# Kernel optimization log

Hardware: AMD Instinct MI355X
Metric: run time of the kernel (lower is better)

Reference implementation:

```python
import jax, jax.numpy as jnp
import numpy as np

N = 100_000
E = 1_600_000
IN_DIM = 3
HID = 64
NUM_CLASSES = 3
BN_EPS = 1e-5


def setup_inputs() -> dict:
    key = jax.random.key(0)
    ks = jax.random.split(key, 16)
    x = jax.random.normal(ks[0], (N, IN_DIM), dtype=jnp.float32)
    row = jax.random.randint(ks[1], (E,), 0, N, dtype=jnp.int32)
    col = jax.random.randint(ks[2], (E,), 0, N, dtype=jnp.int32)
    vals = jax.random.uniform(ks[3], (E,), dtype=jnp.float32)
    # parameters
    W1 = jax.random.normal(ks[4], (IN_DIM, HID), dtype=jnp.float32) / np.sqrt(IN_DIM)
    b1 = jnp.zeros((HID,), jnp.float32)
    W2 = jax.random.normal(ks[5], (HID, HID), dtype=jnp.float32) / np.sqrt(HID)
    b2 = jnp.zeros((HID,), jnp.float32)
    g1 = jnp.ones((HID,), jnp.float32)
    be1 = jnp.zeros((HID,), jnp.float32)
    m1 = jax.random.normal(ks[6], (HID,), dtype=jnp.float32) * 0.1
    v1 = jax.random.uniform(ks[7], (HID,), dtype=jnp.float32) + 0.5
    g2 = jnp.ones((HID,), jnp.float32)
    be2 = jnp.zeros((HID,), jnp.float32)
    m2 = jax.random.normal(ks[8], (HID,), dtype=jnp.float32) * 0.1
    v2 = jax.random.uniform(ks[9], (HID,), dtype=jnp.float32) + 0.5
    Wc = jax.random.normal(ks[10], (2 * HID, NUM_CLASSES), dtype=jnp.float32) / np.sqrt(2 * HID)
    bc = jnp.zeros((NUM_CLASSES,), jnp.float32)
    return dict(x=x, row=row, col=col, vals=vals, W1=W1, b1=b1, g1=g1, be1=be1,
                m1=m1, v1=v1, W2=W2, b2=b2, g2=g2, be2=be2, m2=m2, v2=v2,
                Wc=Wc, bc=bc)


def _spmm(row, col, vals, h):
    # sparse [N,N] @ dense [N,H] via gather + segment_sum
    return jax.ops.segment_sum(vals[:, None] * h[col], row, num_segments=N)


def _bn_eval(h, g, be, m, v):
    return (h - m) * jax.lax.rsqrt(v + BN_EPS) * g + be


def reference(x, row, col, vals, W1, b1, g1, be1, m1, v1,
              W2, b2, g2, be2, m2, v2, Wc, bc):
    h = _spmm(row, col, vals, x @ W1 + b1)          # [N, HID]
    h = jax.nn.relu(_bn_eval(h, g1, be1, m1, v1))   # eval: dropout no-op
    h = _spmm(row, col, vals, h @ W2 + b2)          # [N, HID]
    h = jax.nn.relu(_bn_eval(h, g2, be2, m2, v2))
    g = jnp.concatenate([h.mean(axis=0), h.max(axis=0)], axis=0)  # [2*HID]
    return g @ Wc + bc                               # [NUM_CLASSES]
```

## Files before the change

### kernel.cpp

```cpp
#include <hip/hip_runtime.h>
#include <hip/hip_bf16.h>

#define HID 64
#define BN_EPS 1e-5f
#define BROWS 256
#define MAXB 512
#define BCAP 4608
#define BATCH 4096
#define S2STRIDE 4096

typedef __attribute__((ext_vector_type(8))) short bf16x8;
typedef __attribute__((ext_vector_type(4))) float f32x4;

__global__ __launch_bounds__(512) void zero_bcur_k(int* __restrict__ bcur,
                                                   int* __restrict__ fincnt) {
  bcur[threadIdx.x] = 0;
  if (threadIdx.x == 0) *fincnt = 0;
}

__global__ __launch_bounds__(256) void bucketA_k(
    const int* __restrict__ row, const int* __restrict__ col,
    const float* __restrict__ vals, int* __restrict__ bcur,
    int2* __restrict__ bucketed, int E, int NB) {
  __shared__ int cnt[MAXB];
  __shared__ int scn[MAXB];
  __shared__ int cnt2[MAXB];
  __shared__ int gbase[MAXB];
  __shared__ int2 stg[BATCH];
  __shared__ unsigned short stgb[BATCH];
  int t = threadIdx.x;
  int start = blockIdx.x * BATCH;
  for (int i = t; i < MAXB; i += 256) cnt[i] = 0;
  __syncthreads();
#pragma unroll
  for (int k = 0; k < BATCH / 256; ++k) {
    int i = start + k * 256 + t;
    if (i < E) atomicAdd(&cnt[row[i] >> 8], 1);
  }
  __syncthreads();
  int i0 = t, i1 = t + 256;
  scn[i0] = cnt[i0]; scn[i1] = cnt[i1];
  __syncthreads();
  for (int off = 1; off < 512; off <<= 1) {
    int a0 = (i0 >= off) ? scn[i0 - off] : 0;
    int a1 = (i1 >= off) ? scn[i1 - off] : 0;
    __syncthreads();
    scn[i0] += a0; scn[i1] += a1;
    __syncthreads();
  }
  cnt2[i0] = scn[i0] - cnt[i0];
  cnt2[i1] = scn[i1] - cnt[i1];
  for (int b = t; b < NB; b += 256)
    if (cnt[b] > 0) gbase[b] = atomicAdd(&bcur[b], cnt[b]);
  __syncthreads();
#pragma unroll
  for (int k = 0; k < BATCH / 256; ++k) {
    int i = start + k * 256 + t;
    if (i < E) {
      int r = row[i];
      int b = r >> 8;
      int pos = atomicAdd(&cnt2[b], 1);
      stg[pos] = make_int2(((r & 255) << 17) | col[i], __float_as_int(vals[i]));
      stgb[pos] = (unsigned short)b;
    }
  }
  __syncthreads();
  int m = min(BATCH, E - start);
  for (int s = t; s < m; s += 256) {
    int b = stgb[s];
    int lbase = scn[b] - cnt[b];
    bucketed[(size_t)b * BCAP + gbase[b] + (s - lbase)] = stg[s];
  }
}

__global__ __launch_bounds__(256) void bucketB_k(
    const int2* __restrict__ bucketed, const int* __restrict__ bcnt,
    const float* __restrict__ x,
    const float* __restrict__ W1, const float* __restrict__ b1,
    const float* __restrict__ g, const float* __restrict__ be,
    const float* __restrict__ m, const float* __restrict__ v,
    const float* __restrict__ W2, const float* __restrict__ b2,
    int2* __restrict__ cv, int* __restrict__ rowstart, int* __restrict__ rowend,
    __hip_bfloat16* __restrict__ out, int N) {
  __shared__ int rcnt[BROWS];
  __shared__ int scn[BROWS];
  __shared__ int rcur[BROWS];
  __shared__ float axs[BROWS][4];
  __shared__ int2 stg[BCAP];
  int b = blockIdx.x;
  int t = threadIdx.x;
  int lane = t & 63;
  int wv = t >> 6;
  int li = lane & 15;
  int lk = lane >> 4;
  float A0[16], A1[16], A2[16], A3[16], SS[16];
#pragma unroll
  for (int s = 0; s < 2; ++s)
#pragma unroll
    for (int j = 0; j < 8; ++j) {
      int f = 32 * s + 8 * lk + j;
      float scale = g[f] * rsqrtf(v[f] + BN_EPS);
      float shift = fmaf(-m[f], scale, be[f]);
      int idx = s * 8 + j;
      A0[idx] = scale * W1[0 * HID + f];
      A1[idx] = scale * W1[1 * HID + f];
      A2[idx] = scale * W1[2 * HID + f];
      A3[idx] = scale * b1[f];
      SS[idx] = shift;
    }
  bf16x8 bfr[4][2];
#pragma unroll
  for (int c = 0; c < 4; ++c)
#pragma unroll
    for (int s = 0; s < 2; ++s)
#pragma unroll
      for (int j = 0; j < 8; ++j) {
        int k = 32 * s + 8 * lk + j;
        __hip_bfloat16 hb = __float2bfloat16(W2[k * HID + 16 * c + li]);
        bfr[c][s][j] = *reinterpret_cast<short*>(&hb);
      }
  float b2c[4];
#pragma unroll
  for (int c = 0; c < 4; ++c) b2c[c] = b2[16 * c + li];

  size_t rbase = (size_t)b * BCAP;
  int cnt = bcnt[b];
  int rows = min(BROWS, N - b * BROWS);
  rcnt[t] = 0;
  __syncthreads();
  for (int i = t; i < cnt; i += 256) {
    int2 e = bucketed[rbase + i];
    atomicAdd(&rcnt[e.x >> 17], 1);
  }
  __syncthreads();
  scn[t] = rcnt[t];
  __syncthreads();
  for (int off = 1; off < 256; off <<= 1) {
    int vv = (t >= off) ? scn[t - off] : 0;
    __syncthreads();
    scn[t] += vv;
    __syncthreads();
  }
  int excl = scn[t] - rcnt[t];
  rcur[t] = excl;
  if (t < rows) {
    rowstart[b * BROWS + t] = (int)rbase + excl;
    rowend[b * BROWS + t] = (int)rbase + excl + rcnt[t];
  }
  __syncthreads();
  for (int i = t; i < cnt; i += 256) {
    int2 e = bucketed[rbase + i];
    int pos = atomicAdd(&rcur[e.x >> 17], 1);
    stg[pos] = make_int2(e.x & 0x1FFFF, e.y);
  }
  __syncthreads();
  for (int i = t; i < cnt; i += 256) cv[rbase + i] = stg[i];
  int grp = t >> 4, L = t & 15;
  for (int pass = 0; pass < 16; ++pass) {
    int lrow = pass * 16 + grp;
    int s0 = scn[lrow] - rcnt[lrow];
    int e0 = scn[lrow];
    float a0 = 0.f, a1 = 0.f, a2 = 0.f, a3 = 0.f;
    for (int i2 = s0 + L; i2 < e0; i2 += 16) {
      int2 eg = stg[i2];
      const float* xp = x + 3 * (size_t)eg.x;
      float vv = __int_as_float(eg.y);
      a0 = fmaf(vv, xp[0], a0);
      a1 = fmaf(vv, xp[1], a1);
      a2 = fmaf(vv, xp[2], a2);
      a3 += vv;
    }
#pragma unroll
    for (int msk = 8; msk >= 1; msk >>= 1) {
      a0 += __shfl_xor(a0, msk, 64);
      a1 += __shfl_xor(a1, msk, 64);
      a2 += __shfl_xor(a2, msk, 64);
      a3 += __shfl_xor(a3, msk, 64);
    }
    if (L == 0) {
      axs[lrow][0] = a0; axs[lrow][1] = a1;
      axs[lrow][2] = a2; axs[lrow][3] = a3;
    }
  }
  __syncthreads();
  for (int it = 0; it < 4; ++it) {
    int rb = wv * 4 + it;
    int lrow = rb * 16 + li;
    float a0 = axs[lrow][0], a1 = axs[lrow][1],
          a2 = axs[lrow][2], a3 = axs[lrow][3];
    bf16x8 afr[2];
#pragma unroll
    for (int s = 0; s < 2; ++s)
#pragma unroll
      for (int j = 0; j < 8; ++j) {
        int idx = s * 8 + j;
        float z = fmaf(a0, A0[idx],
                  fmaf(a1, A1[idx],
                  fmaf(a2, A2[idx],
                  fmaf(a3, A3[idx], SS[idx]))));
        float u = fmaxf(z, 0.f);
        __hip_bfloat16 hb = __float2bfloat16(u);
        afr[s][j] = *reinterpret_cast<short*>(&hb);
      }
    f32x4 acc0 = {0.f, 0.f, 0.f, 0.f}, acc1 = {0.f, 0.f, 0.f, 0.f};
    f32x4 acc2 = {0.f, 0.f, 0.f, 0.f}, acc3 = {0.f, 0.f, 0.f, 0.f};
    acc0 = __builtin_amdgcn_mfma_f32_16x16x32_bf16(afr[0], bfr[0][0], acc0, 0, 0, 0);
    acc0 = __builtin_amdgcn_mfma_f32_16x16x32_bf16(afr[1], bfr[0][1], acc0, 0, 0, 0);
    acc1 = __builtin_amdgcn_mfma_f32_16x16x32_bf16(afr[0], bfr[1][0], acc1, 0, 0, 0);
    acc1 = __builtin_amdgcn_mfma_f32_16x16x32_bf16(afr[1], bfr[1][1], acc1, 0, 0, 0);
    acc2 = __builtin_amdgcn_mfma_f32_16x16x32_bf16(afr[0], bfr[2][0], acc2, 0, 0, 0);
    acc2 = __builtin_amdgcn_mfma_f32_16x16x32_bf16(afr[1], bfr[2][1], acc2, 0, 0, 0);
    acc3 = __builtin_amdgcn_mfma_f32_16x16x32_bf16(afr[0], bfr[3][0], acc3, 0, 0, 0);
    acc3 = __builtin_amdgcn_mfma_f32_16x16x32_bf16(afr[1], bfr[3][1], acc3, 0, 0, 0);
#pragma unroll
    for (int r = 0; r < 4; ++r) {
      int orow = b * BROWS + rb * 16 + 4 * lk + r;
      if (orow < N) {
        size_t ob = (size_t)orow * HID + li;
        out[ob + 0]  = __float2bfloat16(acc0[r] + b2c[0]);
        out[ob + 16] = __float2bfloat16(acc1[r] + b2c[1]);
        out[ob + 32] = __float2bfloat16(acc2[r] + b2c[2]);
        out[ob + 48] = __float2bfloat16(acc3[r] + b2c[3]);
      }
    }
  }
}

__global__ __launch_bounds__(256) void spmm2_pool_k(
    const int* __restrict__ rowstart, const int* __restrict__ rowend,
    const int2* __restrict__ cv,
    const __hip_bfloat16* __restrict__ hb,
    const float* __restrict__ g, const float* __restrict__ be,
    const float* __restrict__ m, const float* __restrict__ v,
    float* __restrict__ pS, float* __restrict__ pM, int N) {
  int lane = threadIdx.x & 63;
  int wid = threadIdx.x >> 6;
  int grp = lane >> 3;
  int gl = lane & 7;
  int base = grp << 3;
  float scl[8], shf[8];
#pragma unroll
  for (int j = 0; j < 8; ++j) {
    int f = gl * 8 + j;
    float sc = g[f] * rsqrtf(v[f] + BN_EPS);
    scl[j] = sc;
    shf[j] = fmaf(-m[f], sc, be[f]);
  }
  const uint4* __restrict__ h4 = (const uint4*)hb;
  float psum[8] = {0.f,0.f,0.f,0.f,0.f,0.f,0.f,0.f};
  float pmax[8] = {0.f,0.f,0.f,0.f,0.f,0.f,0.f,0.f};
  int rowstep = gridDim.x * 32;
  for (int r = blockIdx.x * 32 + wid * 8 + grp; r < N; r += rowstep) {
    int s = rowstart[r], e = rowend[r];
    float acc[8] = {0.f,0.f,0.f,0.f,0.f,0.f,0.f,0.f};
    for (int i = s; i < e; i += 8) {
      int take = e - i; if (take > 8) take = 8;
      int2 my = cv[i + (gl < take ? gl : take - 1)];
      int cj[8]; float vj[8];
#pragma unroll
      for (int j = 0; j < 8; ++j) {
        cj[j] = __shfl(my.x, base + j, 64);
        float vv = __uint_as_float((uint)__shfl(my.y, base + j, 64));
        vj[j] = (j < take) ? vv : 0.f;
      }
      uint4 hv[8];
#pragma unroll
      for (int j = 0; j < 8; ++j) hv[j] = h4[(size_t)cj[j] * 8 + gl];
#pragma unroll
      for (int j = 0; j < 8; ++j) {
        acc[0] = fmaf(vj[j], __uint_as_float(hv[j].x << 16), acc[0]);
        acc[1] = fmaf(vj[j], __uint_as_float(hv[j].x & 0xffff0000u), acc[1]);
        acc[2] = fmaf(vj[j], __uint_as_float(hv[j].y << 16), acc[2]);
        acc[3] = fmaf(vj[j], __uint_as_float(hv[j].y & 0xffff0000u), acc[3]);
        acc[4] = fmaf(vj[j], __uint_as_float(hv[j].z << 16), acc[4]);
        acc[5] = fmaf(vj[j], __uint_as_float(hv[j].z & 0xffff0000u), acc[5]);
        acc[6] = fmaf(vj[j], __uint_as_float(hv[j].w << 16), acc[6]);
        acc[7] = fmaf(vj[j], __uint_as_float(hv[j].w & 0xffff0000u), acc[7]);
      }
    }
#pragma unroll
    for (int j = 0; j < 8; ++j) {
      float hvl = fmaxf(fmaf(acc[j], scl[j], shf[j]), 0.f);
      psum[j] += hvl;
      pmax[j] = fmaxf(pmax[j], hvl);
    }
  }
  __shared__ float ls[32][HID], lm[32][HID];
  int slot = wid * 8 + grp;
#pragma unroll
  for (int j = 0; j < 8; ++j) {
    ls[slot][gl * 8 + j] = psum[j];
    lm[slot][gl * 8 + j] = pmax[j];
  }
  __syncthreads();
  int t = threadIdx.x;
  if (t < HID) {
    float s32 = 0.f, m32 = 0.f;
#pragma unroll
    for (int kk = 0; kk < 32; ++kk) {
      s32 += ls[kk][t];
      m32 = fmaxf(m32, lm[kk][t]);
    }
    pS[(size_t)t * S2STRIDE + blockIdx.x] = s32;
    pM[(size_t)t * S2STRIDE + blockIdx.x] = m32;
  }
}

__global__ __launch_bounds__(256) void pool_final_k(
    const float* __restrict__ pS, const float* __restrict__ pM,
    float* __restrict__ gsum, float* __restrict__ gmaxf,
    int* __restrict__ fincnt,
    const float* __restrict__ Wc, const float* __restrict__ bc,
    float* __restrict__ out, float invN, int nblk) {
  int f = blockIdx.x;
  int t = threadIdx.x;
  float s = 0.f, m = 0.f;
  for (int j = t; j < nblk; j += 256) {
    s += pS[(size_t)f * S2STRIDE + j];
    m = fmaxf(m, pM[(size_t)f * S2STRIDE + j]);
  }
#pragma unroll
  for (int msk = 32; msk >= 1; msk >>= 1) {
    s += __shfl_xor(s, msk, 64);
    m = fmaxf(m, __shfl_xor(m, msk, 64));
  }
  __shared__ float ws_[4], wm_[4];
  __shared__ int amLast;
  if ((t & 63) == 0) { ws_[t >> 6] = s; wm_[t >> 6] = m; }
  __syncthreads();
  if (t == 0) {
    s = ws_[0] + ws_[1] + ws_[2] + ws_[3];
    m = fmaxf(fmaxf(wm_[0], wm_[1]), fmaxf(wm_[2], wm_[3]));
    atomicExch(&gsum[f], s);
    atomicExch(&gmaxf[f], m);
    __threadfence();
    int prev = atomicAdd(fincnt, 1);
    amLast = (prev == HID - 1);
  }
  __syncthreads();
  if (!amLast) return;
  __shared__ float red[128 * 3];
  int j = t;
  if (j < 128) {
    float gj = (j < HID) ? atomicAdd(&gsum[j], 0.f) * invN
                         : atomicAdd(&gmaxf[j - HID], 0.f);
#pragma unroll
    for (int c = 0; c < 3; ++c) red[j * 3 + c] = gj * Wc[j * 3 + c];
  }
  __syncthreads();
  for (int off = 64; off >= 1; off >>= 1) {
    if (j < off) {
#pragma unroll
      for (int c = 0; c < 3; ++c) red[j * 3 + c] += red[(j + off) * 3 + c];
    }
    __syncthreads();
  }
  if (j < 3) out[j] = red[j] + bc[j];
}

extern "C" void kernel_launch(void* const* d_in, const int* in_sizes, int n_in,
                              void* d_out, int out_size, void* d_ws, size_t ws_size,
                              hipStream_t stream) {
  const float* x    = (const float*)d_in[0];
  const int*   row  = (const int*)d_in[1];
  const int*   col  = (const int*)d_in[2];
  const float* vals = (const float*)d_in[3];
  const float* W1   = (const float*)d_in[4];
  const float* b1   = (const float*)d_in[5];
  const float* g1   = (const float*)d_in[6];
  const float* be1  = (const float*)d_in[7];
  const float* m1   = (const float*)d_in[8];
  const float* v1   = (const float*)d_in[9];
  const float* W2   = (const float*)d_in[10];
  const float* b2   = (const float*)d_in[11];
  const float* g2   = (const float*)d_in[12];
  const float* be2  = (const float*)d_in[13];
  const float* m2   = (const float*)d_in[14];
  const float* v2   = (const float*)d_in[15];
  const float* Wc   = (const float*)d_in[16];
  const float* bc   = (const float*)d_in[17];
  float* out = (float*)d_out;

  const int N = in_sizes[0] / 3;
  const int E = in_sizes[1];
  const int NB = (N + BROWS - 1) / BROWS;
  const int S2G = (N + 31) / 32;

  __hip_bfloat16* wsA = (__hip_bfloat16*)d_ws;
  int2* bucketed = (int2*)(wsA + (size_t)N * HID);
  int2* cv = bucketed + (size_t)MAXB * BCAP;
  int* rowstart = (int*)(cv + (size_t)MAXB * BCAP);
  int* rowend = rowstart + N;
  int* bcur = rowend + N;
  int* fincnt = bcur + MAXB;
  float* pS = (float*)(fincnt + 2);
  float* pM = pS + (size_t)HID * S2STRIDE;
  float* gsum = pM + (size_t)HID * S2STRIDE;
  float* gmaxf = gsum + HID;

  zero_bcur_k<<<1, 512, 0, stream>>>(bcur, fincnt);
  bucketA_k<<<(E + BATCH - 1) / BATCH, 256, 0, stream>>>(row, col, vals, bcur, bucketed, E, NB);
  bucketB_k<<<NB, 256, 0, stream>>>(bucketed, bcur, x,
                                    W1, b1, g1, be1, m1, v1, W2, b2,
                                    cv, rowstart, rowend, wsA, N);

  spmm2_pool_k<<<S2G, 256, 0, stream>>>(rowstart, rowend, cv, wsA, g2, be2, m2, v2, pS, pM, N);
  pool_final_k<<<HID, 256, 0, stream>>>(pS, pM, gsum, gmaxf, fincnt,
                                        Wc, bc, out, 1.0f / (float)N, S2G);
}
```

Baseline: 107.0 us.

## Sort rows by degree before second SpMM to balance per-wave work

Measured after the change: 396.5 us. 271% more time.

```diff
diff --git a/kernel.cpp b/kernel.cpp
--- a/kernel.cpp
+++ b/kernel.cpp
@@ -8,13 +8,16 @@
 #define BCAP 4608
 #define BATCH 4096
 #define S2STRIDE 4096
+#define DBINS 64
 
 typedef __attribute__((ext_vector_type(8))) short bf16x8;
 typedef __attribute__((ext_vector_type(4))) float f32x4;
 
 __global__ __launch_bounds__(512) void zero_bcur_k(int* __restrict__ bcur,
-                                                   int* __restrict__ fincnt) {
+                                                   int* __restrict__ fincnt,
+                                                   int* __restrict__ dbin) {
   bcur[threadIdx.x] = 0;
+  if (threadIdx.x < DBINS) dbin[threadIdx.x] = 0;
   if (threadIdx.x == 0) *fincnt = 0;
 }
 
@@ -81,10 +84,12 @@
     const float* __restrict__ m, const float* __restrict__ v,
     const float* __restrict__ W2, const float* __restrict__ b2,
     int2* __restrict__ cv, int* __restrict__ rowstart, int* __restrict__ rowend,
+    int* __restrict__ dbin,
     __hip_bfloat16* __restrict__ out, int N) {
   __shared__ int rcnt[BROWS];
   __shared__ int scn[BROWS];
   __shared__ int rcur[BROWS];
+  __shared__ int lbin[DBINS];
   __shared__ float axs[BROWS][4];
   __shared__ int2 stg[BCAP];
   int b = blockIdx.x;
@@ -127,6 +132,7 @@
   int cnt = bcnt[b];
   int rows = min(BROWS, N - b * BROWS);
   rcnt[t] = 0;
+  if (t < DBINS) lbin[t] = 0;
   __syncthreads();
   for (int i = t; i < cnt; i += 256) {
     int2 e = bucketed[rbase + i];
@@ -146,6 +152,7 @@
   if (t < rows) {
     rowstart[b * BROWS + t] = (int)rbase + excl;
     rowend[b * BROWS + t] = (int)rbase + excl + rcnt[t];
+    atomicAdd(&lbin[min(rcnt[t], DBINS - 1)], 1);
   }
   __syncthreads();
   for (int i = t; i < cnt; i += 256) {
@@ -153,6 +160,7 @@
     int pos = atomicAdd(&rcur[e.x >> 17], 1);
     stg[pos] = make_int2(e.x & 0x1FFFF, e.y);
   }
+  if (t < DBINS && lbin[t]) atomicAdd(&dbin[t], lbin[t]);
   __syncthreads();
   for (int i = t; i < cnt; i += 256) cv[rbase + i] = stg[i];
   int grp = t >> 4, L = t & 15;
@@ -226,7 +234,26 @@
   }
 }
 
+__global__ __launch_bounds__(DBINS) void dscan_k(const int* __restrict__ dbin,
+                                                 int* __restrict__ dcur) {
+  int t = threadIdx.x;
+  int s = 0;
+  for (int i = 0; i < t; ++i) s += dbin[i];
+  dcur[t] = s;
+}
+
+__global__ __launch_bounds__(256) void dperm_k(
+    const int* __restrict__ rowstart, const int* __restrict__ rowend,
+    int* __restrict__ dcur, int* __restrict__ perm, int N) {
+  int r = blockIdx.x * 256 + threadIdx.x;
+  if (r >= N) return;
+  int deg = rowend[r] - rowstart[r];
+  int pos = atomicAdd(&dcur[min(deg, DBINS - 1)], 1);
+  perm[pos] = r;
+}
+
 __global__ __launch_bounds__(256) void spmm2_pool_k(
+    const int* __restrict__ perm,
     const int* __restrict__ rowstart, const int* __restrict__ rowend,
     const int2* __restrict__ cv,
     const __hip_bfloat16* __restrict__ hb,
@@ -250,7 +277,8 @@
   float psum[8] = {0.f,0.f,0.f,0.f,0.f,0.f,0.f,0.f};
   float pmax[8] = {0.f,0.f,0.f,0.f,0.f,0.f,0.f,0.f};
   int rowstep = gridDim.x * 32;
-  for (int r = blockIdx.x * 32 + wid * 8 + grp; r < N; r += rowstep) {
+  for (int ridx = blockIdx.x * 32 + wid * 8 + grp; ridx < N; ridx += rowstep) {
+    int r = perm[ridx];
     int s = rowstart[r], e = rowend[r];
     float acc[8] = {0.f,0.f,0.f,0.f,0.f,0.f,0.f,0.f};
     for (int i = s; i < e; i += 8) {
@@ -391,20 +419,26 @@
   int2* cv = bucketed + (size_t)MAXB * BCAP;
   int* rowstart = (int*)(cv + (size_t)MAXB * BCAP);
   int* rowend = rowstart + N;
-  int* bcur = rowend + N;
+  int* perm = rowend + N;
+  int* bcur = perm + N;
   int* fincnt = bcur + MAXB;
-  float* pS = (float*)(fincnt + 2);
+  int* dbin = fincnt + 2;
+  int* dcur = dbin + DBINS;
+  float* pS = (float*)(dcur + DBINS);
   float* pM = pS + (size_t)HID * S2STRIDE;
   float* gsum = pM + (size_t)HID * S2STRIDE;
   float* gmaxf = gsum + HID;
 
-  zero_bcur_k<<<1, 512, 0, stream>>>(bcur, fincnt);
+  zero_bcur_k<<<1, 512, 0, stream>>>(bcur, fincnt, dbin);
   bucketA_k<<<(E + BATCH - 1) / BATCH, 256, 0, stream>>>(row, col, vals, bcur, bucketed, E, NB);
   bucketB_k<<<NB, 256, 0, stream>>>(bucketed, bcur, x,
                                     W1, b1, g1, be1, m1, v1, W2, b2,
-                                    cv, rowstart, rowend, wsA, N);
-
-  spmm2_pool_k<<<S2G, 256, 0, stream>>>(rowstart, rowend, cv, wsA, g2, be2, m2, v2, pS, pM, N);
+                                    cv, rowstart, rowend, dbin, wsA, N);
+  dscan_k<<<1, DBINS, 0, stream>>>(dbin, dcur);
+  dperm_k<<<(N + 255) / 256, 256, 0, stream>>>(rowstart, rowend, dcur, perm, N);
+
+  spmm2_pool_k<<<S2G, 256, 0, stream>>>(perm, rowstart, rowend, cv, wsA,
+                                        g2, be2, m2, v2, pS, pM, N);
   pool_final_k<<<HID, 256, 0, stream>>>(pS, pM, gsum, gmaxf, fincnt,
                                         Wc, bc, out, 1.0f / (float)N, S2G);
 }
```
